# Kernel optimization log

Hardware: AMD Instinct MI355X
Metric: run time of the kernel (lower is better)

## Reference

```python
import jax, jax.numpy as jnp
import numpy as np
import math

KEY_SIZE = 64

def setup_inputs() -> dict:
    key = jax.random.key(0)
    kq, kk, kv, km = jax.random.split(key, 4)
    B, H, S, Dk, Dv = 4, 12, 2048, 64, 64
    Q = jax.random.normal(kq, (B, H, S, Dk), dtype=jnp.float32)
    K = jax.random.normal(kk, (B, H, S, Dk), dtype=jnp.float32)
    V = jax.random.normal(kv, (B, H, S, Dv), dtype=jnp.float32)
    mask_out = (jax.random.uniform(km, (B, H, 1, S)) < 0.9).astype(jnp.float32)
    return {"Q": Q, "K": K, "V": V, "mask_out": mask_out}

def reference(Q, K, V, mask_out):
    scale = math.sqrt(KEY_SIZE)
    # [B,H,Sq,Sk] scores
    scores = jnp.einsum('bhqd,bhkd->bhqk', Q, K) / scale
    attn = jax.nn.softmax(scores, axis=-1)
    attn = mask_out * attn  # post-softmax multiplicative mask (dropout=0)
    return jnp.einsum('bhqk,bhkv->bhqv', attn, V)
```

## Files before the change

kernel.cpp:

```cpp
#include <hip/hip_runtime.h>


typedef _Float16 f16x8 __attribute__((ext_vector_type(8)));
typedef _Float16 f16x4 __attribute__((ext_vector_type(4)));
typedef _Float16 f16x2 __attribute__((ext_vector_type(2)));
typedef float    f32x4 __attribute__((ext_vector_type(4)));

#define SEQ  2048
#define DIM  64
#define KT   64
#define LDSP 72
#define NIT  (SEQ / KT)

__device__ inline f16x8 cvt8(float4 a, float4 b) {
    return (f16x8){(_Float16)a.x,(_Float16)a.y,(_Float16)a.z,(_Float16)a.w,
                   (_Float16)b.x,(_Float16)b.y,(_Float16)b.z,(_Float16)b.w};
}
__device__ inline f16x8 cvt8s(float4 a, float4 b, float s) {
    return (f16x8){(_Float16)(a.x*s),(_Float16)(a.y*s),(_Float16)(a.z*s),(_Float16)(a.w*s),
                   (_Float16)(b.x*s),(_Float16)(b.y*s),(_Float16)(b.z*s),(_Float16)(b.w*s)};
}

__global__ __launch_bounds__(256, 3)
void fa_kernel(const float* __restrict__ Q, const float* __restrict__ K,
               const float* __restrict__ V, const float* __restrict__ Mask,
               float* __restrict__ Out)
{
    __shared__ _Float16 Kld[KT][LDSP];
    __shared__ _Float16 Vt[DIM][LDSP];

    const int bx    = blockIdx.x;
    const int head  = bx % 48;
    const int qtile = bx / 48;
    const int tid   = threadIdx.x;
    const int wave  = tid >> 6;
    const int lane  = tid & 63;
    const int quad  = lane >> 4;
    const int r     = lane & 15;

    const size_t hoff = (size_t)head * SEQ * DIM;
    const float* Qh = Q + hoff;
    const float* Kh = K + hoff;
    const float* Vh = V + hoff;
    const float* Mh = Mask + (size_t)head * SEQ;
    float* Oh = Out + hoff;

    const int qbase = qtile * 128 + wave * 32;
    const float c = 0.18033688011112042f;

    f16x8 qf[2][2];
    #pragma unroll
    for (int t = 0; t < 2; ++t) {
        const float* qrow = Qh + (size_t)(qbase + t * 16 + r) * DIM;
        #pragma unroll
        for (int kb = 0; kb < 2; ++kb) {
            const float4* p4 = (const float4*)(qrow + kb * 32 + quad * 8);
            qf[t][kb] = cvt8s(p4[0], p4[1], c);
        }
    }

    f32x4 o[4][2];
    float lsum[2] = {0.f, 0.f};
    #pragma unroll
    for (int d = 0; d < 4; ++d)
        #pragma unroll
        for (int t = 0; t < 2; ++t) o[d][t] = (f32x4){0.f, 0.f, 0.f, 0.f};

    const int skey = tid >> 2;
    const int sdb  = (tid & 3) * 16;
    const int vk0  = (tid & 31) * 2;
    const int vdb  = (tid >> 5) * 8;

    float4 kr0, kr1, kr2, kr3, va0, va1, vb0, vb1;
    float mk0, mk1;
    auto load_tile = [&](int kbase) {
        const float4* kg = (const float4*)(Kh + (size_t)(kbase + skey) * DIM + sdb);
        kr0 = kg[0]; kr1 = kg[1]; kr2 = kg[2]; kr3 = kg[3];
        const float4* vg0 = (const float4*)(Vh + (size_t)(kbase + vk0) * DIM + vdb);
        const float4* vg1 = (const float4*)(Vh + (size_t)(kbase + vk0 + 1) * DIM + vdb);
        va0 = vg0[0]; va1 = vg0[1];
        vb0 = vg1[0]; vb1 = vg1[1];
        mk0 = Mh[kbase + vk0]; mk1 = Mh[kbase + vk0 + 1];
    };
    load_tile(0);

    for (int kbi = 0; kbi < NIT; ++kbi) {
        __syncthreads();
        *(f16x8*)&Kld[skey][sdb]     = cvt8(kr0, kr1);
        *(f16x8*)&Kld[skey][sdb + 8] = cvt8(kr2, kr3);
        {
            float va[8] = {va0.x, va0.y, va0.z, va0.w, va1.x, va1.y, va1.z, va1.w};
            float vb[8] = {vb0.x, vb0.y, vb0.z, vb0.w, vb1.x, vb1.y, vb1.z, vb1.w};
            #pragma unroll
            for (int j = 0; j < 8; ++j) {
                f16x2 w = {(_Float16)(va[j] * mk0), (_Float16)(vb[j] * mk1)};
                *(f16x2*)&Vt[vdb + j][vk0] = w;
            }
        }
        __syncthreads();

        if (kbi + 1 < NIT) load_tile((kbi + 1) * KT);

        f16x4 pf[4][2];
        #pragma unroll
        for (int kt = 0; kt < 4; ++kt) {
            f16x8 kf0 = *(const f16x8*)&Kld[kt * 16 + r][0 * 32 + quad * 8];
            f16x8 kf1 = *(const f16x8*)&Kld[kt * 16 + r][1 * 32 + quad * 8];
            #pragma unroll
            for (int t = 0; t < 2; ++t) {
                f32x4 acc = (f32x4){-8.f, -8.f, -8.f, -8.f};
                acc = __builtin_amdgcn_mfma_f32_16x16x32_f16(kf0, qf[t][0], acc, 0, 0, 0);
                acc = __builtin_amdgcn_mfma_f32_16x16x32_f16(kf1, qf[t][1], acc, 0, 0, 0);
                float p0 = __builtin_amdgcn_exp2f(acc[0]);
                float p1 = __builtin_amdgcn_exp2f(acc[1]);
                float p2 = __builtin_amdgcn_exp2f(acc[2]);
                float p3 = __builtin_amdgcn_exp2f(acc[3]);
                lsum[t] += (p0 + p1) + (p2 + p3);
                pf[kt][t] = (f16x4){(_Float16)p0, (_Float16)p1,
                                    (_Float16)p2, (_Float16)p3};
            }
        }

        #pragma unroll
        for (int d = 0; d < 4; ++d) {
            #pragma unroll
            for (int kt = 0; kt < 4; ++kt) {
                f16x4 vfrag = *(const f16x4*)&Vt[d * 16 + r][kt * 16 + quad * 4];
                o[d][0] = __builtin_amdgcn_mfma_f32_16x16x16f16(vfrag, pf[kt][0], o[d][0], 0, 0, 0);
                o[d][1] = __builtin_amdgcn_mfma_f32_16x16x16f16(vfrag, pf[kt][1], o[d][1], 0, 0, 0);
            }
        }
    }

    #pragma unroll
    for (int t = 0; t < 2; ++t) {
        float l = lsum[t];
        l += __shfl_xor(l, 16);
        l += __shfl_xor(l, 32);
        float inv = 1.0f / l;
        const size_t rowoff = (size_t)(qbase + t * 16 + r) * DIM;
        #pragma unroll
        for (int d = 0; d < 4; ++d) {
            float4 v = {o[d][t][0] * inv, o[d][t][1] * inv,
                        o[d][t][2] * inv, o[d][t][3] * inv};
            *(float4*)&Oh[rowoff + d * 16 + quad * 4] = v;
        }
    }
}

extern "C" void kernel_launch(void* const* d_in, const int* in_sizes, int n_in,
                              void* d_out, int out_size, void* d_ws, size_t ws_size,
                              hipStream_t stream) {
    const float* Q = (const float*)d_in[0];
    const float* K = (const float*)d_in[1];
    const float* V = (const float*)d_in[2];
    const float* M = (const float*)d_in[3];
    float* O = (float*)d_out;
    dim3 grid(768), block(256);
    hipLaunchKernelGGL(fa_kernel, grid, block, 0, stream, Q, K, V, M, O);
}
```

Before: 181.9 us.

## Use 16x16x32 MFMA for PV and compute row sums via ones-MFMA

```diff
diff --git a/kernel.cpp b/kernel.cpp
--- a/kernel.cpp
+++ b/kernel.cpp
@@ -59,15 +59,21 @@
         }
     }
 
-    f32x4 o[4][2];
-    float lsum[2] = {0.f, 0.f};
+    f32x4 o[4][2], ol[2];
     #pragma unroll
     for (int d = 0; d < 4; ++d)
         #pragma unroll
         for (int t = 0; t < 2; ++t) o[d][t] = (f32x4){0.f, 0.f, 0.f, 0.f};
+    ol[0] = (f32x4){0.f, 0.f, 0.f, 0.f};
+    ol[1] = (f32x4){0.f, 0.f, 0.f, 0.f};
+
+    const f16x8 ones8 = {(_Float16)1.f,(_Float16)1.f,(_Float16)1.f,(_Float16)1.f,
+                         (_Float16)1.f,(_Float16)1.f,(_Float16)1.f,(_Float16)1.f};
 
     const int skey = tid >> 2;
     const int sdb  = (tid & 3) * 16;
+    const int srow = ((skey >> 5) << 5) + (((skey & 7) < 4) ? 0 : 16)
+                   + (((skey & 31) >> 3) << 2) + (skey & 3);
     const int vk0  = (tid & 31) * 2;
     const int vdb  = (tid >> 5) * 8;
 
@@ -86,8 +92,8 @@
 
     for (int kbi = 0; kbi < NIT; ++kbi) {
         __syncthreads();
-        *(f16x8*)&Kld[skey][sdb]     = cvt8(kr0, kr1);
-        *(f16x8*)&Kld[skey][sdb + 8] = cvt8(kr2, kr3);
+        *(f16x8*)&Kld[srow][sdb]     = cvt8(kr0, kr1);
+        *(f16x8*)&Kld[srow][sdb + 8] = cvt8(kr2, kr3);
         {
             float va[8] = {va0.x, va0.y, va0.z, va0.w, va1.x, va1.y, va1.z, va1.w};
             float vb[8] = {vb0.x, vb0.y, vb0.z, vb0.w, vb1.x, vb1.y, vb1.z, vb1.w};
@@ -101,43 +107,47 @@
 
         if (kbi + 1 < NIT) load_tile((kbi + 1) * KT);
 
-        f16x4 pf[4][2];
+        f16x8 bfrag[2][2];
         #pragma unroll
-        for (int kt = 0; kt < 4; ++kt) {
-            f16x8 kf0 = *(const f16x8*)&Kld[kt * 16 + r][0 * 32 + quad * 8];
-            f16x8 kf1 = *(const f16x8*)&Kld[kt * 16 + r][1 * 32 + quad * 8];
+        for (int g = 0; g < 2; ++g) {
             #pragma unroll
-            for (int t = 0; t < 2; ++t) {
-                f32x4 acc = (f32x4){-8.f, -8.f, -8.f, -8.f};
-                acc = __builtin_amdgcn_mfma_f32_16x16x32_f16(kf0, qf[t][0], acc, 0, 0, 0);
-                acc = __builtin_amdgcn_mfma_f32_16x16x32_f16(kf1, qf[t][1], acc, 0, 0, 0);
-                float p0 = __builtin_amdgcn_exp2f(acc[0]);
-                float p1 = __builtin_amdgcn_exp2f(acc[1]);
-                float p2 = __builtin_amdgcn_exp2f(acc[2]);
-                float p3 = __builtin_amdgcn_exp2f(acc[3]);
-                lsum[t] += (p0 + p1) + (p2 + p3);
-                pf[kt][t] = (f16x4){(_Float16)p0, (_Float16)p1,
-                                    (_Float16)p2, (_Float16)p3};
+            for (int u = 0; u < 2; ++u) {
+                const int ti = g * 2 + u;
+                f16x8 kf0 = *(const f16x8*)&Kld[ti * 16 + r][quad * 8];
+                f16x8 kf1 = *(const f16x8*)&Kld[ti * 16 + r][32 + quad * 8];
+                #pragma unroll
+                for (int t = 0; t < 2; ++t) {
+                    f32x4 acc = (f32x4){-8.f, -8.f, -8.f, -8.f};
+                    acc = __builtin_amdgcn_mfma_f32_16x16x32_f16(kf0, qf[t][0], acc, 0, 0, 0);
+                    acc = __builtin_amdgcn_mfma_f32_16x16x32_f16(kf1, qf[t][1], acc, 0, 0, 0);
+                    #pragma unroll
+                    for (int i = 0; i < 4; ++i)
+                        bfrag[g][t][u * 4 + i] =
+                            (_Float16)__builtin_amdgcn_exp2f(acc[i]);
+                }
             }
+        }
+
+        #pragma unroll
+        for (int g = 0; g < 2; ++g) {
+            ol[0] = __builtin_amdgcn_mfma_f32_16x16x32_f16(ones8, bfrag[g][0], ol[0], 0, 0, 0);
+            ol[1] = __builtin_amdgcn_mfma_f32_16x16x32_f16(ones8, bfrag[g][1], ol[1], 0, 0, 0);
         }
 
         #pragma unroll
         for (int d = 0; d < 4; ++d) {
             #pragma unroll
-            for (int kt = 0; kt < 4; ++kt) {
-                f16x4 vfrag = *(const f16x4*)&Vt[d * 16 + r][kt * 16 + quad * 4];
-                o[d][0] = __builtin_amdgcn_mfma_f32_16x16x16f16(vfrag, pf[kt][0], o[d][0], 0, 0, 0);
-                o[d][1] = __builtin_amdgcn_mfma_f32_16x16x16f16(vfrag, pf[kt][1], o[d][1], 0, 0, 0);
+            for (int g = 0; g < 2; ++g) {
+                f16x8 vfrag = *(const f16x8*)&Vt[d * 16 + r][g * 32 + quad * 8];
+                o[d][0] = __builtin_amdgcn_mfma_f32_16x16x32_f16(vfrag, bfrag[g][0], o[d][0], 0, 0, 0);
+                o[d][1] = __builtin_amdgcn_mfma_f32_16x16x32_f16(vfrag, bfrag[g][1], o[d][1], 0, 0, 0);
             }
         }
     }
 
     #pragma unroll
     for (int t = 0; t < 2; ++t) {
-        float l = lsum[t];
-        l += __shfl_xor(l, 16);
-        l += __shfl_xor(l, 32);
-        float inv = 1.0f / l;
+        float inv = 1.0f / ol[t][0];
         const size_t rowoff = (size_t)(qbase + t * 16 + r) * DIM;
         #pragma unroll
         for (int d = 0; d < 4; ++d) {
```

New measurement: 184.4 us. About the same (+1.4%).

## Double key tile to 128 and interleave next-tile conversion with MFMA work

Applied to the files above, without the earlier changes.

```diff
diff --git a/kernel.cpp b/kernel.cpp
--- a/kernel.cpp
+++ b/kernel.cpp
@@ -6,11 +6,12 @@
 typedef _Float16 f16x2 __attribute__((ext_vector_type(2)));
 typedef float    f32x4 __attribute__((ext_vector_type(4)));
 
-#define SEQ  2048
-#define DIM  64
-#define KT   64
-#define LDSP 72
-#define NIT  (SEQ / KT)
+#define SEQ   2048
+#define DIM   64
+#define KT    128
+#define NIT   (SEQ / KT)
+#define LDSK  72
+#define LDSV  136
 
 __device__ inline f16x8 cvt8(float4 a, float4 b) {
     return (f16x8){(_Float16)a.x,(_Float16)a.y,(_Float16)a.z,(_Float16)a.w,
@@ -26,8 +27,8 @@
                const float* __restrict__ V, const float* __restrict__ Mask,
                float* __restrict__ Out)
 {
-    __shared__ _Float16 Kld[KT][LDSP];
-    __shared__ _Float16 Vt[DIM][LDSP];
+    __shared__ _Float16 Kld[KT][LDSK];
+    __shared__ _Float16 Vt[DIM][LDSV];
 
     const int bx    = blockIdx.x;
     const int head  = bx % 48;
@@ -66,70 +67,106 @@
         #pragma unroll
         for (int t = 0; t < 2; ++t) o[d][t] = (f32x4){0.f, 0.f, 0.f, 0.f};
 
-    const int skey = tid >> 2;
-    const int sdb  = (tid & 3) * 16;
-    const int vk0  = (tid & 31) * 2;
-    const int vdb  = (tid >> 5) * 8;
+    const int skey  = tid >> 1;
+    const int sdb   = (tid & 1) * 32;
+    const int vpair = tid & 63;
+    const int vdb   = (tid >> 6) * 16;
 
-    float4 kr0, kr1, kr2, kr3, va0, va1, vb0, vb1;
+    float4 fk0, fk1, fk2, fk3, fk4, fk5, fk6, fk7;
+    float4 fa0, fa1, fa2, fa3, fb0, fb1, fb2, fb3;
     float mk0, mk1;
+    f16x8 kk0, kk1, kk2, kk3;
+    f16x2 vv0, vv1, vv2, vv3, vv4, vv5, vv6, vv7,
+          vv8, vv9, vv10, vv11, vv12, vv13, vv14, vv15;
+
     auto load_tile = [&](int kbase) {
         const float4* kg = (const float4*)(Kh + (size_t)(kbase + skey) * DIM + sdb);
-        kr0 = kg[0]; kr1 = kg[1]; kr2 = kg[2]; kr3 = kg[3];
-        const float4* vg0 = (const float4*)(Vh + (size_t)(kbase + vk0) * DIM + vdb);
-        const float4* vg1 = (const float4*)(Vh + (size_t)(kbase + vk0 + 1) * DIM + vdb);
-        va0 = vg0[0]; va1 = vg0[1];
-        vb0 = vg1[0]; vb1 = vg1[1];
-        mk0 = Mh[kbase + vk0]; mk1 = Mh[kbase + vk0 + 1];
+        fk0 = kg[0]; fk1 = kg[1]; fk2 = kg[2]; fk3 = kg[3];
+        fk4 = kg[4]; fk5 = kg[5]; fk6 = kg[6]; fk7 = kg[7];
+        const float4* vg0 = (const float4*)(Vh + (size_t)(kbase + 2 * vpair) * DIM + vdb);
+        const float4* vg1 = (const float4*)(Vh + (size_t)(kbase + 2 * vpair + 1) * DIM + vdb);
+        fa0 = vg0[0]; fa1 = vg0[1]; fa2 = vg0[2]; fa3 = vg0[3];
+        fb0 = vg1[0]; fb1 = vg1[1]; fb2 = vg1[2]; fb3 = vg1[3];
+        const float2 mm = *(const float2*)&Mh[kbase + 2 * vpair];
+        mk0 = mm.x; mk1 = mm.y;
     };
-    load_tile(0);
+    auto cvtK = [&]() {
+        kk0 = cvt8(fk0, fk1); kk1 = cvt8(fk2, fk3);
+        kk2 = cvt8(fk4, fk5); kk3 = cvt8(fk6, fk7);
+    };
+    auto cvtV = [&]() {
+        vv0  = (f16x2){(_Float16)(fa0.x*mk0), (_Float16)(fb0.x*mk1)};
+        vv1  = (f16x2){(_Float16)(fa0.y*mk0), (_Float16)(fb0.y*mk1)};
+        vv2  = (f16x2){(_Float16)(fa0.z*mk0), (_Float16)(fb0.z*mk1)};
+        vv3  = (f16x2){(_Float16)(fa0.w*mk0), (_Float16)(fb0.w*mk1)};
+        vv4  = (f16x2){(_Float16)(fa1.x*mk0), (_Float16)(fb1.x*mk1)};
+        vv5  = (f16x2){(_Float16)(fa1.y*mk0), (_Float16)(fb1.y*mk1)};
+        vv6  = (f16x2){(_Float16)(fa1.z*mk0), (_Float16)(fb1.z*mk1)};
+        vv7  = (f16x2){(_Float16)(fa1.w*mk0), (_Float16)(fb1.w*mk1)};
+        vv8  = (f16x2){(_Float16)(fa2.x*mk0), (_Float16)(fb2.x*mk1)};
+        vv9  = (f16x2){(_Float16)(fa2.y*mk0), (_Float16)(fb2.y*mk1)};
+        vv10 = (f16x2){(_Float16)(fa2.z*mk0), (_Float16)(fb2.z*mk1)};
+        vv11 = (f16x2){(_Float16)(fa2.w*mk0), (_Float16)(fb2.w*mk1)};
+        vv12 = (f16x2){(_Float16)(fa3.x*mk0), (_Float16)(fb3.x*mk1)};
+        vv13 = (f16x2){(_Float16)(fa3.y*mk0), (_Float16)(fb3.y*mk1)};
+        vv14 = (f16x2){(_Float16)(fa3.z*mk0), (_Float16)(fb3.z*mk1)};
+        vv15 = (f16x2){(_Float16)(fa3.w*mk0), (_Float16)(fb3.w*mk1)};
+    };
+    auto stage = [&]() {
+        *(f16x8*)&Kld[skey][sdb]      = kk0;
+        *(f16x8*)&Kld[skey][sdb + 8]  = kk1;
+        *(f16x8*)&Kld[skey][sdb + 16] = kk2;
+        *(f16x8*)&Kld[skey][sdb + 24] = kk3;
+        const int vc = 2 * vpair;
+        *(f16x2*)&Vt[vdb +  0][vc] = vv0;  *(f16x2*)&Vt[vdb +  1][vc] = vv1;
+        *(f16x2*)&Vt[vdb +  2][vc] = vv2;  *(f16x2*)&Vt[vdb +  3][vc] = vv3;
+        *(f16x2*)&Vt[vdb +  4][vc] = vv4;  *(f16x2*)&Vt[vdb +  5][vc] = vv5;
+        *(f16x2*)&Vt[vdb +  6][vc] = vv6;  *(f16x2*)&Vt[vdb +  7][vc] = vv7;
+        *(f16x2*)&Vt[vdb +  8][vc] = vv8;  *(f16x2*)&Vt[vdb +  9][vc] = vv9;
+        *(f16x2*)&Vt[vdb + 10][vc] = vv10; *(f16x2*)&Vt[vdb + 11][vc] = vv11;
+        *(f16x2*)&Vt[vdb + 12][vc] = vv12; *(f16x2*)&Vt[vdb + 13][vc] = vv13;
+        *(f16x2*)&Vt[vdb + 14][vc] = vv14; *(f16x2*)&Vt[vdb + 15][vc] = vv15;
+    };
+
+    auto qkpv = [&](int kt) {
+        f16x8 kf0 = *(const f16x8*)&Kld[kt * 16 + r][quad * 8];
+        f16x8 kf1 = *(const f16x8*)&Kld[kt * 16 + r][32 + quad * 8];
+        f16x4 pf[2];
+        #pragma unroll
+        for (int t = 0; t < 2; ++t) {
+            f32x4 acc = (f32x4){-8.f, -8.f, -8.f, -8.f};
+            acc = __builtin_amdgcn_mfma_f32_16x16x32_f16(kf0, qf[t][0], acc, 0, 0, 0);
+            acc = __builtin_amdgcn_mfma_f32_16x16x32_f16(kf1, qf[t][1], acc, 0, 0, 0);
+            float p0 = __builtin_amdgcn_exp2f(acc[0]);
+            float p1 = __builtin_amdgcn_exp2f(acc[1]);
+            float p2 = __builtin_amdgcn_exp2f(acc[2]);
+            float p3 = __builtin_amdgcn_exp2f(acc[3]);
+            lsum[t] += (p0 + p1) + (p2 + p3);
+            pf[t] = (f16x4){(_Float16)p0, (_Float16)p1, (_Float16)p2, (_Float16)p3};
+        }
+        #pragma unroll
+        for (int d = 0; d < 4; ++d) {
+            f16x4 vfrag = *(const f16x4*)&Vt[d * 16 + r][kt * 16 + quad * 4];
+            o[d][0] = __builtin_amdgcn_mfma_f32_16x16x16f16(vfrag, pf[0], o[d][0], 0, 0, 0);
+            o[d][1] = __builtin_amdgcn_mfma_f32_16x16x16f16(vfrag, pf[1], o[d][1], 0, 0, 0);
+        }
+    };
+
+    load_tile(0); cvtK(); cvtV();
 
     for (int kbi = 0; kbi < NIT; ++kbi) {
         __syncthreads();
-        *(f16x8*)&Kld[skey][sdb]     = cvt8(kr0, kr1);
-        *(f16x8*)&Kld[skey][sdb + 8] = cvt8(kr2, kr3);
-        {
-            float va[8] = {va0.x, va0.y, va0.z, va0.w, va1.x, va1.y, va1.z, va1.w};
-            float vb[8] = {vb0.x, vb0.y, vb0.z, vb0.w, vb1.x, vb1.y, vb1.z, vb1.w};
-            #pragma unroll
-            for (int j = 0; j < 8; ++j) {
-                f16x2 w = {(_Float16)(va[j] * mk0), (_Float16)(vb[j] * mk1)};
-                *(f16x2*)&Vt[vdb + j][vk0] = w;
-            }
-        }
+        stage();
         __syncthreads();
 
-        if (kbi + 1 < NIT) load_tile((kbi + 1) * KT);
+        const bool pre = (kbi + 1 < NIT);
+        if (pre) load_tile((kbi + 1) * KT);
 
-        f16x4 pf[4][2];
-        #pragma unroll
-        for (int kt = 0; kt < 4; ++kt) {
-            f16x8 kf0 = *(const f16x8*)&Kld[kt * 16 + r][0 * 32 + quad * 8];
-            f16x8 kf1 = *(const f16x8*)&Kld[kt * 16 + r][1 * 32 + quad * 8];
-            #pragma unroll
-            for (int t = 0; t < 2; ++t) {
-                f32x4 acc = (f32x4){-8.f, -8.f, -8.f, -8.f};
-                acc = __builtin_amdgcn_mfma_f32_16x16x32_f16(kf0, qf[t][0], acc, 0, 0, 0);
-                acc = __builtin_amdgcn_mfma_f32_16x16x32_f16(kf1, qf[t][1], acc, 0, 0, 0);
-                float p0 = __builtin_amdgcn_exp2f(acc[0]);
-                float p1 = __builtin_amdgcn_exp2f(acc[1]);
-                float p2 = __builtin_amdgcn_exp2f(acc[2]);
-                float p3 = __builtin_amdgcn_exp2f(acc[3]);
-                lsum[t] += (p0 + p1) + (p2 + p3);
-                pf[kt][t] = (f16x4){(_Float16)p0, (_Float16)p1,
-                                    (_Float16)p2, (_Float16)p3};
-            }
-        }
-
-        #pragma unroll
-        for (int d = 0; d < 4; ++d) {
-            #pragma unroll
-            for (int kt = 0; kt < 4; ++kt) {
-                f16x4 vfrag = *(const f16x4*)&Vt[d * 16 + r][kt * 16 + quad * 4];
-                o[d][0] = __builtin_amdgcn_mfma_f32_16x16x16f16(vfrag, pf[kt][0], o[d][0], 0, 0, 0);
-                o[d][1] = __builtin_amdgcn_mfma_f32_16x16x16f16(vfrag, pf[kt][1], o[d][1], 0, 0, 0);
-            }
-        }
+        qkpv(0); qkpv(1);
+        if (pre) cvtK();
+        qkpv(2); qkpv(3); qkpv(4); qkpv(5);
+        if (pre) cvtV();
+        qkpv(6); qkpv(7);
     }
 
     #pragma unroll
```

After: 526.3 us. +189.3%, slower.
